# Performance work log

Measured on AMD Instinct MI355X. Metric: run time of the kernel, lower is better.

The kernel has to match this reference:

```python
import jax, jax.numpy as jnp
import numpy as np

T, N, C, S = 512, 32, 5000, 100
BLANK = 0
NEG = -1e30  # log-space 'zero'


def setup_inputs() -> dict:
    key = jax.random.key(0)
    k1, k2, k3 = jax.random.split(key, 3)
    logits = jax.random.normal(k1, (T, N, C), dtype=jnp.float32)
    log_probs = jax.nn.log_softmax(logits, axis=-1)  # CTC expects log-probs
    targets = jax.random.randint(k2, (N, S), 1, C)   # labels never equal blank(=0)
    input_lengths = jnp.full((N,), T, dtype=jnp.int32)
    target_lengths = jax.random.randint(k3, (N,), S // 2, S + 1).astype(jnp.int32)
    return {"log_probs": log_probs, "targets": targets,
            "input_lengths": input_lengths, "target_lengths": target_lengths}


def _logsumexp3(a, b, c):
    m = jnp.maximum(jnp.maximum(a, b), c)
    return m + jnp.log(jnp.exp(a - m) + jnp.exp(b - m) + jnp.exp(c - m))


def _ctc_loss(log_probs, targets, input_lengths, target_lengths, blank=BLANK):
    Tm, Nb, Cc = log_probs.shape
    Sm = targets.shape[1]
    L = 2 * Sm + 1  # extended (blank-interleaved) label lattice width

    # extended targets: [blank, t0, blank, t1, ..., blank]  -> shape [N, L]
    ext = jnp.full((Nb, L), blank, dtype=targets.dtype)
    ext = ext.at[:, 1::2].set(targets)
    is_label = (jnp.arange(L) % 2 == 1)
    ext_prev2 = jnp.concatenate(
        [jnp.full((Nb, 2), -1, dtype=ext.dtype), ext[:, :-2]], axis=1)
    allow_skip = is_label[None, :] & (ext != ext_prev2)          # [N, L]
    pos_mask = jnp.arange(L)[None, :] < (2 * target_lengths + 1)[:, None]

    def emit(lp_t):  # lp_t: [N, C] -> [N, L] gather of label log-probs
        return jnp.take_along_axis(lp_t, ext, axis=1)

    # init alpha at t=0
    e0 = emit(log_probs[0])
    alpha0 = jnp.full((Nb, L), NEG, dtype=log_probs.dtype)
    alpha0 = alpha0.at[:, 0].set(e0[:, 0])
    alpha0 = alpha0.at[:, 1].set(jnp.where(target_lengths > 0, e0[:, 1], NEG))
    alpha0 = jnp.where(pos_mask, alpha0, NEG)

    neg1 = jnp.full((Nb, 1), NEG, dtype=log_probs.dtype)
    neg2 = jnp.full((Nb, 2), NEG, dtype=log_probs.dtype)

    def step(alpha, xs):
        lp_t, t = xs
        a1 = jnp.concatenate([neg1, alpha[:, :-1]], axis=1)
        a2 = jnp.where(allow_skip,
                       jnp.concatenate([neg2, alpha[:, :-2]], axis=1), NEG)
        new = _logsumexp3(alpha, a1, a2) + emit(lp_t)
        new = jnp.where(pos_mask, new, NEG)
        active = (t < input_lengths)[:, None]  # freeze alpha past input length
        return jnp.where(active, new, alpha), None

    alpha, _ = jax.lax.scan(step, alpha0,
                            (log_probs[1:], jnp.arange(1, Tm)))

    # total log-likelihood: last blank + last label states
    last = (2 * target_lengths).astype(jnp.int32)
    a_blank = jnp.take_along_axis(alpha, last[:, None], axis=1)[:, 0]
    a_label = jnp.take_along_axis(alpha, jnp.maximum(last - 1, 0)[:, None], axis=1)[:, 0]
    m = jnp.maximum(a_blank, a_label)
    ll = m + jnp.log(jnp.exp(a_blank - m) + jnp.exp(a_label - m))
    loss = -ll
    # zero_infinity=True: zero out infinite losses
    loss = jnp.where(jnp.isfinite(loss) & (loss < 1e29), loss, 0.0)
    # reduction='mean': divide by target_lengths (clamped to 1), then batch mean
    loss = loss / jnp.maximum(target_lengths, 1).astype(loss.dtype)
    return jnp.mean(loss)


def reference(log_probs, targets, input_lengths, target_lengths):
    return _ctc_loss(log_probs, targets, input_lengths, target_lengths)
```

## Files before the change

kernel.cpp:

```cpp
#include <hip/hip_runtime.h>
#include <cstdint>
#include <cmath>

#define Tt   512
#define Nb   32
#define Cc   5000
#define Sm   100
#define NEGV (-1e30f)
#define LOG2E 1.4426950408889634f
#define LN2   0.6931471805599453f
#define TCH  8

#if __has_builtin(__builtin_amdgcn_exp2f)
#define EXP2F(x) __builtin_amdgcn_exp2f(x)
#else
#define EXP2F(x) exp2f(x)
#endif
#if __has_builtin(__builtin_amdgcn_logf)
#define LOG2F(x) __builtin_amdgcn_logf(x)
#else
#define LOG2F(x) log2f(x)
#endif

__device__ __forceinline__ float lse2_l2(float a, float b) {
    float m = fmaxf(a, b);
    return m + LOG2F(1.0f + EXP2F(fminf(a, b) - m));
}
__device__ __forceinline__ float lse3_l2(float a, float b, float c) {
    float m   = fmaxf(fmaxf(a, b), c);
    float mid = __builtin_amdgcn_fmed3f(a, b, c);
    float lo  = fminf(fminf(a, b), c);
    return m + LOG2F(1.0f + EXP2F(mid - m) + EXP2F(lo - m));
}

__global__ __launch_bounds__(128, 1)
void ctc_gather_kernel(const float* __restrict__ lp,
                       const int*   __restrict__ tgt,
                       float*       __restrict__ em2,
                       float*       __restrict__ bl)
{
    const int bid = blockIdx.x;
    const int n   = bid >> 6;
    const int t0  = (bid & 63) * TCH;
    const int j   = threadIdx.x;

    float* dst = em2 + (((size_t)n * Tt + t0) << 7) + j;

    if (j < Sm) {
        const int e = tgt[n * Sm + j];
        const float* src = lp + (size_t)n * Cc + e;
        float v[TCH];
#pragma unroll
        for (int k = 0; k < TCH; ++k)
            v[k] = src[(size_t)(t0 + k) * (Nb * Cc)];
#pragma unroll
        for (int k = 0; k < TCH; ++k)
            dst[k << 7] = v[k] * LOG2E;
    } else {
#pragma unroll
        for (int k = 0; k < TCH; ++k)
            dst[k << 7] = NEGV;
        if (j < Sm + TCH) {
            int k = j - Sm;
            bl[n * Tt + t0 + k] =
                lp[(size_t)(t0 + k) * (Nb * Cc) + (size_t)n * Cc] * LOG2E;
        }
    }
}

__global__ __launch_bounds__(64, 1)
void ctc_alpha_wave_kernel(const float* __restrict__ em2,
                           const float* __restrict__ bl,
                           const int*   __restrict__ tgt,
                           const int*   __restrict__ ilen,
                           const int*   __restrict__ tlen,
                           float*       __restrict__ per_loss)
{
    const int n = blockIdx.x;
    const int i = threadIdx.x;

    const int tl = tlen[n];
    const int il = ilen[n];

    const int j1 = 2 * i, j3 = 2 * i + 1;
    bool s1 = false, s3 = false;
    if (j1 >= 1 && j1 < Sm) s1 = (tgt[n * Sm + j1] != tgt[n * Sm + j1 - 1]);
    if (j3 < Sm)            s3 = (tgt[n * Sm + j3] != tgt[n * Sm + j3 - 1]);

    const float2* e2 = (const float2*)em2 + ((size_t)n << 15);
    const float*  bn = bl + n * Tt;

    const int pull = (i > 0 ? i - 1 : 0) << 2;

    float2 E0 = e2[i];
    float a0 = (i == 0)           ? bn[0] : NEGV;
    float a1 = (i == 0 && tl > 0) ? E0.x  : NEGV;
    float a2 = NEGV;
    float a3 = NEGV;

    constexpr int PF = 8;
    float2 ebuf[PF];
#pragma unroll
    for (int k = 0; k < PF; ++k) {
        int t = 1 + k;
        ebuf[k] = (t < Tt) ? e2[(t << 6) + i] : make_float2(NEGV, NEGV);
    }

    for (int tb = 1; tb < Tt; tb += PF) {
#pragma unroll
        for (int k = 0; k < PF; ++k) {
            const int t = tb + k;
            if (t < Tt) {
                float2 e  = ebuf[k];
                float  eb = bn[t];
                int    tp = t + PF;
                if (tp < Tt) ebuf[k] = e2[(tp << 6) + i];

                float p3  = __int_as_float(
                    __builtin_amdgcn_ds_bpermute(pull, __float_as_int(a3)));
                float am0 = (i > 0) ? p3 : NEGV;

                float n0 = lse2_l2(a0, am0)                   + eb;
                float n1 = lse3_l2(a1, a0, s1 ? p3 : NEGV)    + e.x;
                float n2 = lse2_l2(a2, a1)                    + eb;
                float n3 = lse3_l2(a3, a2, s3 ? a1 : NEGV)    + e.y;

                if (t < il) {
                    a0 = n0; a1 = n1; a2 = n2; a3 = n3;
                }
            }
        }
    }

    const int lb = 2 * tl;
    const int lv = (lb - 1 >= 0) ? lb - 1 : 0;

    int   cb = lb & 3;
    float vb = (cb == 0) ? a0 : (cb == 1) ? a1 : (cb == 2) ? a2 : a3;
    float ab = __shfl(vb, lb >> 2);
    int   cl = lv & 3;
    float vl = (cl == 0) ? a0 : (cl == 1) ? a1 : (cl == 2) ? a2 : a3;
    float al = __shfl(vl, lv >> 2);

    if (i == 0) {
        float m    = fmaxf(ab, al);
        float ll2  = m + LOG2F(EXP2F(ab - m) + EXP2F(al - m));
        float loss = -ll2 * LN2;
        if (!(isfinite(loss) && loss < 1e29f)) loss = 0.0f;
        int   d    = (tl >= 1) ? tl : 1;
        per_loss[n] = loss / (float)d;
    }
}

__global__ void ctc_finalize_kernel(const float* __restrict__ per_loss,
                                    float* __restrict__ out)
{
    int i = threadIdx.x;
    float v = (i < Nb) ? per_loss[i] : 0.0f;
#pragma unroll
    for (int off = 32; off > 0; off >>= 1)
        v += __shfl_down(v, off, 64);
    if (i == 0) out[0] = v * (1.0f / Nb);
}

extern "C" void kernel_launch(void* const* d_in, const int* in_sizes, int n_in,
                              void* d_out, int out_size, void* d_ws, size_t ws_size,
                              hipStream_t stream)
{
    const float* lp   = (const float*)d_in[0];
    const int*   tgt  = (const int*)  d_in[1];
    const int*   ilen = (const int*)  d_in[2];
    const int*   tlen = (const int*)  d_in[3];
    float*       out  = (float*)d_out;

    float* per_loss = (float*)d_ws;
    float* bl       = (float*)((char*)d_ws + 256);
    float* em2      = (float*)((char*)d_ws + 256 + (size_t)Nb * Tt * 4);

    ctc_gather_kernel<<<Nb * (Tt / TCH), 128, 0, stream>>>(lp, tgt, em2, bl);
    ctc_alpha_wave_kernel<<<Nb, 64, 0, stream>>>(em2, bl, tgt, ilen, tlen, per_loss);
    ctc_finalize_kernel<<<1, 64, 0, stream>>>(per_loss, out);
}
```

Baseline: 491.9 us.

## Fold blank emissions into the emission table and drop the finalize kernel

The gather kernel now writes the blank log-prob into slot 100 of each per-timestep emission row, so the alpha kernel no longer reads a separate blank array. Instead it broadcasts that value with readlane from lane 50's float2. The per-sequence losses are accumulated with an atomicAdd into the output, which the gather kernel zeroes, removing the third kernel launch. This removes one dependent global load per timestep in the serial recurrence and one launch. In exchange the summation order becomes nondeterministic.

```diff
diff --git a/kernel.cpp b/kernel.cpp
--- a/kernel.cpp
+++ b/kernel.cpp
@@ -37,17 +37,19 @@
 void ctc_gather_kernel(const float* __restrict__ lp,
                        const int*   __restrict__ tgt,
                        float*       __restrict__ em2,
-                       float*       __restrict__ bl)
+                       float*       __restrict__ out)
 {
     const int bid = blockIdx.x;
     const int n   = bid >> 6;
     const int t0  = (bid & 63) * TCH;
     const int j   = threadIdx.x;
 
+    if (bid == 0 && j == 127) out[0] = 0.0f;
+
     float* dst = em2 + (((size_t)n * Tt + t0) << 7) + j;
 
-    if (j < Sm) {
-        const int e = tgt[n * Sm + j];
+    if (j <= Sm) {
+        const int e = (j < Sm) ? tgt[n * Sm + j] : 0;
         const float* src = lp + (size_t)n * Cc + e;
         float v[TCH];
 #pragma unroll
@@ -60,21 +62,15 @@
 #pragma unroll
         for (int k = 0; k < TCH; ++k)
             dst[k << 7] = NEGV;
-        if (j < Sm + TCH) {
-            int k = j - Sm;
-            bl[n * Tt + t0 + k] =
-                lp[(size_t)(t0 + k) * (Nb * Cc) + (size_t)n * Cc] * LOG2E;
-        }
     }
 }
 
 __global__ __launch_bounds__(64, 1)
 void ctc_alpha_wave_kernel(const float* __restrict__ em2,
-                           const float* __restrict__ bl,
                            const int*   __restrict__ tgt,
                            const int*   __restrict__ ilen,
                            const int*   __restrict__ tlen,
-                           float*       __restrict__ per_loss)
+                           float*       __restrict__ out)
 {
     const int n = blockIdx.x;
     const int i = threadIdx.x;
@@ -88,23 +84,22 @@
     if (j3 < Sm)            s3 = (tgt[n * Sm + j3] != tgt[n * Sm + j3 - 1]);
 
     const float2* e2 = (const float2*)em2 + ((size_t)n << 15);
-    const float*  bn = bl + n * Tt;
 
     const int pull = (i > 0 ? i - 1 : 0) << 2;
 
     float2 E0 = e2[i];
-    float a0 = (i == 0)           ? bn[0] : NEGV;
-    float a1 = (i == 0 && tl > 0) ? E0.x  : NEGV;
+    float b0 = __int_as_float(
+        __builtin_amdgcn_readlane(__float_as_int(E0.x), 50));
+    float a0 = (i == 0)           ? b0   : NEGV;
+    float a1 = (i == 0 && tl > 0) ? E0.x : NEGV;
     float a2 = NEGV;
     float a3 = NEGV;
 
     constexpr int PF = 8;
     float2 ebuf[PF];
 #pragma unroll
-    for (int k = 0; k < PF; ++k) {
-        int t = 1 + k;
-        ebuf[k] = (t < Tt) ? e2[(t << 6) + i] : make_float2(NEGV, NEGV);
-    }
+    for (int k = 0; k < PF; ++k)
+        ebuf[k] = e2[((1 + k) << 6) + i];
 
     for (int tb = 1; tb < Tt; tb += PF) {
 #pragma unroll
@@ -112,9 +107,11 @@
             const int t = tb + k;
             if (t < Tt) {
                 float2 e  = ebuf[k];
-                float  eb = bn[t];
                 int    tp = t + PF;
                 if (tp < Tt) ebuf[k] = e2[(tp << 6) + i];
+
+                float eb = __int_as_float(
+                    __builtin_amdgcn_readlane(__float_as_int(e.x), 50));
 
                 float p3  = __int_as_float(
                     __builtin_amdgcn_ds_bpermute(pull, __float_as_int(a3)));
@@ -148,19 +145,8 @@
         float loss = -ll2 * LN2;
         if (!(isfinite(loss) && loss < 1e29f)) loss = 0.0f;
         int   d    = (tl >= 1) ? tl : 1;
-        per_loss[n] = loss / (float)d;
+        atomicAdd(out, loss / ((float)d * (float)Nb));
     }
-}
-
-__global__ void ctc_finalize_kernel(const float* __restrict__ per_loss,
-                                    float* __restrict__ out)
-{
-    int i = threadIdx.x;
-    float v = (i < Nb) ? per_loss[i] : 0.0f;
-#pragma unroll
-    for (int off = 32; off > 0; off >>= 1)
-        v += __shfl_down(v, off, 64);
-    if (i == 0) out[0] = v * (1.0f / Nb);
 }
 
 extern "C" void kernel_launch(void* const* d_in, const int* in_sizes, int n_in,
@@ -173,11 +159,8 @@
     const int*   tlen = (const int*)  d_in[3];
     float*       out  = (float*)d_out;
 
-    float* per_loss = (float*)d_ws;
-    float* bl       = (float*)((char*)d_ws + 256);
-    float* em2      = (float*)((char*)d_ws + 256 + (size_t)Nb * Tt * 4);
+    float* em2 = (float*)d_ws;
 
-    ctc_gather_kernel<<<Nb * (Tt / TCH), 128, 0, stream>>>(lp, tgt, em2, bl);
-    ctc_alpha_wave_kernel<<<Nb, 64, 0, stream>>>(em2, bl, tgt, ilen, tlen, per_loss);
-    ctc_finalize_kernel<<<1, 64, 0, stream>>>(per_loss, out);
+    ctc_gather_kernel<<<Nb * (Tt / TCH), 128, 0, stream>>>(lp, tgt, em2, out);
+    ctc_alpha_wave_kernel<<<Nb, 64, 0, stream>>>(em2, tgt, ilen, tlen, out);
 }
```

Measured after the change: 480.1 us. -2.4%, faster.
